# Kernel optimization log

Hardware: AMD Instinct MI355X
Metric: run time of the kernel (lower is better)

## Reference

```python
import jax, jax.numpy as jnp
import numpy as np

B, D, E = 16384, 2048, 16
MIN_K, MAX_K = 1, 4
H = D // 2  # hidden width of similarity/routing MLPs
TOP20 = int(0.2 * D)  # static: int(0.2 * x.shape[-1])


def _lin_init(k, fan_in, shape):
    bound = 1.0 / np.sqrt(fan_in)
    return jax.random.uniform(k, shape, jnp.float32, -bound, bound)


def setup_inputs() -> dict:
    key = jax.random.key(0)
    ks = jax.random.split(key, 16)
    return {
        'x': jax.random.normal(ks[0], (B, D), jnp.float32),
        'expert_patterns': jax.random.normal(ks[1], (E, D), jnp.float32),
        # similarity_network: Linear(D, D//2) -> ReLU -> Linear(D//2, E)
        'Ws1': _lin_init(ks[2], D, (D, H)), 'bs1': _lin_init(ks[3], D, (H,)),
        'Ws2': _lin_init(ks[4], H, (H, E)), 'bs2': _lin_init(ks[5], H, (E,)),
        # routing_network: Linear(D+E, D//2) -> ReLU -> (Dropout eval) -> Linear(D//2, E) -> Softmax
        'Wr1': _lin_init(ks[6], D + E, (D + E, H)), 'br1': _lin_init(ks[7], D + E, (H,)),
        'Wr2': _lin_init(ks[8], H, (H, E)), 'br2': _lin_init(ks[9], H, (E,)),
        # k_predictor: Linear(6,16) -> ReLU -> Linear(16,1) -> Sigmoid
        'Wk1': _lin_init(ks[10], 6, (6, 16)), 'bk1': _lin_init(ks[11], 6, (16,)),
        'Wk2': _lin_init(ks[12], 16, (16, 1)), 'bk2': _lin_init(ks[13], 16, (1,)),
    }


def _feature_analysis(x):
    mean = jnp.mean(x, axis=-1, keepdims=True)
    var_u = jnp.var(x, axis=-1, ddof=1)  # torch.var is unbiased
    std = jnp.sqrt(var_u[:, None] + 1e-8)
    skew = jnp.mean(((x - mean) / std) ** 3, axis=-1)
    ax = jnp.abs(x)
    sorted_ax = -jnp.sort(-ax, axis=-1)  # descending
    total = jnp.sum(sorted_ax, axis=-1)
    top = jnp.sum(sorted_ax[:, :TOP20], axis=-1)
    # stacked in DynamicTopKSelector order: sparsity,variance,magnitude,norm,skewness,concentration
    stats = jnp.stack([
        jnp.mean((x == 0).astype(jnp.float32), axis=-1),
        var_u,
        jnp.max(ax, axis=-1),
        jnp.linalg.norm(x, axis=-1),
        skew,
        top / (total + 1e-8),
    ], axis=-1)  # [B, 6]
    return stats


def _lower_median(v):
    # torch.median returns the lower of two middle elements for even n
    n = v.shape[0]
    return jnp.sort(v)[(n - 1) // 2]


def reference(x, expert_patterns, Ws1, bs1, Ws2, bs2, Wr1, br1, Wr2, br2, Wk1, bk1, Wk2, bk2):
    stats = _feature_analysis(x)  # [B, 6]
    # expert specialization
    sims = x @ expert_patterns.T                                  # [B, E]
    spec = jax.nn.relu(x @ Ws1 + bs1) @ Ws2 + bs2                 # [B, E]
    spec_scores = jax.nn.sigmoid(sims + spec)
    # routing network (dropout inactive in eval)
    ri = jnp.concatenate([x, spec_scores], axis=-1)               # [B, D+E]
    probs = jax.nn.softmax(jax.nn.relu(ri @ Wr1 + br1) @ Wr2 + br2, axis=-1)
    # dynamic top-k (host-side scalar in torch -> static-shape pad/mask here)
    k_ratio = jax.nn.sigmoid(jax.nn.relu(stats @ Wk1 + bk1) @ Wk2 + bk2)[:, 0]
    k_values = MIN_K + (MAX_K - MIN_K) * k_ratio
    k = jnp.clip(jnp.floor(_lower_median(k_values)).astype(jnp.int32), MIN_K, MAX_K)
    k = jax.lax.stop_gradient(k)
    topk_probs, topk_idx = jax.lax.top_k(probs, MAX_K)            # [B, MAX_K]
    mask = jnp.arange(MAX_K) < k                                  # first k slots active
    gates = jax.nn.softmax(jnp.where(mask, topk_probs, -1e30), axis=-1)
    return gates, topk_idx, probs, stats
```

## Files before the change

kernel.cpp:

```cpp
#include <hip/hip_runtime.h>
#include <hip/hip_bf16.h>

typedef unsigned short u16;
typedef __attribute__((ext_vector_type(8))) short bf16x8;
typedef __attribute__((ext_vector_type(4))) float f32x4;

#define BB 16384
#define DD 2048
#define KEXT 2112
#define HH 1024
#define EE 16
#define TOPN 409

__device__ __forceinline__ u16 f2bf(float f) {
    union { float f; unsigned u; } c; c.f = f;
    unsigned r = c.u + 0x7fffu + ((c.u >> 16) & 1u);
    return (u16)(r >> 16);
}
__device__ __forceinline__ float bf2f(u16 h) {
    union { unsigned u; float f; } c; c.u = ((unsigned)h) << 16; return c.f;
}

__device__ __forceinline__ void ld16_lds(const void* g, void* l) {
    __builtin_amdgcn_global_load_lds(
        (const __attribute__((address_space(1))) unsigned int*)g,
        (__attribute__((address_space(3))) unsigned int*)l, 16, 0, 0);
}

__global__ __launch_bounds__(256)
void prep_t(const float* __restrict__ Ws1, const float* __restrict__ Wr1,
            u16* __restrict__ w1t, u16* __restrict__ wr1h, u16* __restrict__ wr1l,
            const float* __restrict__ Ws2, const float* __restrict__ Wr2,
            const float* __restrict__ pat,
            u16* __restrict__ w2t1, u16* __restrict__ wr2th, u16* __restrict__ wr2tl,
            u16* __restrict__ patTh, u16* __restrict__ patTl)
{
    __shared__ float tile[64][65];
    const int kt = blockIdx.x;
    const int nt = blockIdx.y;
    const int mat = blockIdx.z;
    const int t = threadIdx.x;
    if (mat == 2) {
        int idx = (kt * 16 + nt) * 256 + t;
        if (idx < EE * HH) {
            int e = idx / HH, n = idx % HH;
            w2t1[idx] = f2bf(Ws2[(size_t)n * EE + e]);
            float v = Wr2[(size_t)n * EE + e];
            u16 h = f2bf(v);
            wr2th[idx] = h;
            wr2tl[idx] = f2bf(v - bf2f(h));
        }
        if (idx < EE * DD) {
            float v = pat[idx];
            u16 h = f2bf(v);
            patTh[idx] = h;
            patTl[idx] = f2bf(v - bf2f(h));
        }
        return;
    }
    if (mat == 0 && kt >= 32) return;
    const int k0 = kt * 64, n0 = nt * 64;
    const float* src = mat ? Wr1 : Ws1;
    const int kmax = mat ? (DD + EE) : DD;
    #pragma unroll
    for (int i = 0; i < 16; ++i) {
        int e = i * 256 + t;
        int r = e >> 6, c = e & 63;
        float v = (k0 + r < kmax) ? src[(size_t)(k0 + r) * HH + n0 + c] : 0.0f;
        tile[r][c] = v;
    }
    __syncthreads();
    #pragma unroll
    for (int i = 0; i < 16; ++i) {
        int e = i * 256 + t;
        int rn = e >> 6, ck = e & 63;
        float v = tile[ck][rn];
        size_t oidx = (size_t)(n0 + rn) * KEXT + k0 + ck;
        if (mat == 0) {
            w1t[oidx] = f2bf(v);
        } else {
            u16 h = f2bf(v);
            wr1h[oidx] = h;
            wr1l[oidx] = f2bf(v - bf2f(h));
        }
    }
}

__global__ __launch_bounds__(256)
void stats_kernel(const float* __restrict__ x,
                  const float* __restrict__ Wk1, const float* __restrict__ bk1,
                  const float* __restrict__ Wk2, const float* __restrict__ bk2,
                  float* __restrict__ stats_out, u16* __restrict__ xh, u16* __restrict__ xl,
                  unsigned* __restrict__ kflags)
{
    const int wid = threadIdx.x >> 6;
    const int lane = threadIdx.x & 63;
    const int row = blockIdx.x * 4 + wid;
    const float* xr = x + (size_t)row * DD;

    float v[32];
    #pragma unroll
    for (int s = 0; s < 8; ++s) {
        float4 a = *(const float4*)(xr + s * 256 + lane * 4);
        v[s*4+0]=a.x; v[s*4+1]=a.y; v[s*4+2]=a.z; v[s*4+3]=a.w;
    }

    u16* ph = xh + (size_t)row * KEXT;
    u16* pl = xl + (size_t)row * KEXT;
    #pragma unroll
    for (int s = 0; s < 8; ++s) {
        union { u16 a[4]; unsigned long long q; } H, L;
        #pragma unroll
        for (int c = 0; c < 4; ++c) {
            float f = v[s*4+c];
            u16 h = f2bf(f);
            H.a[c] = h; L.a[c] = f2bf(f - bf2f(h));
        }
        *(unsigned long long*)(ph + s*256 + lane*4) = H.q;
        *(unsigned long long*)(pl + s*256 + lane*4) = L.q;
    }
    ph[DD + lane] = 0;
    pl[DD + lane] = 0;

    float s1 = 0;
    #pragma unroll
    for (int j = 0; j < 32; ++j) s1 += v[j];
    #pragma unroll
    for (int off = 32; off >= 1; off >>= 1) s1 += __shfl_xor(s1, off);
    const float mean = s1 * (1.0f/2048.0f);

    float s2=0, s3=0, sa=0, sq=0, zc=0, mx=0;
    #pragma unroll
    for (int j = 0; j < 32; ++j) {
        float d = v[j] - mean;
        s2 += d*d; s3 += d*d*d;
        float av = fabsf(v[j]);
        sa += av; sq += v[j]*v[j];
        mx = fmaxf(mx, av);
        zc += (v[j] == 0.0f) ? 1.0f : 0.0f;
    }
    #pragma unroll
    for (int off = 32; off >= 1; off >>= 1) {
        s2 += __shfl_xor(s2, off);
        s3 += __shfl_xor(s3, off);
        sa += __shfl_xor(sa, off);
        sq += __shfl_xor(sq, off);
        zc += __shfl_xor(zc, off);
        mx = fmaxf(mx, __shfl_xor(mx, off));
    }

    #pragma unroll
    for (int j = 0; j < 32; ++j) v[j] = fabsf(v[j]);

    unsigned lo = 0, hi = 0x7F800000u;
    while (lo < hi) {
        unsigned mid = (lo + hi) >> 1;
        float midf = __uint_as_float(mid);
        unsigned cnt = 0;
        #pragma unroll
        for (int j = 0; j < 32; ++j)
            cnt += (unsigned)__popcll(__ballot(v[j] > midf));
        if (cnt < TOPN) hi = mid; else lo = mid + 1;
    }
    const float T = __uint_as_float(lo);

    float cg = 0, sg = 0;
    #pragma unroll
    for (int j = 0; j < 32; ++j) {
        if (v[j] > T) { cg += 1.0f; sg += v[j]; }
    }
    #pragma unroll
    for (int off = 32; off >= 1; off >>= 1) { cg += __shfl_xor(cg, off); sg += __shfl_xor(sg, off); }

    if (lane == 0) {
        float top = sg + ((float)TOPN - cg) * T;
        float var_u = s2 * (1.0f/2047.0f);
        float stdv = sqrtf(var_u + 1e-8f);
        float st0 = zc * (1.0f/2048.0f);
        float st1 = var_u;
        float st2 = mx;
        float st3 = sqrtf(sq);
        float st4 = (s3 * (1.0f/2048.0f)) / (stdv*stdv*stdv);
        float st5 = top / (sa + 1e-8f);
        float* so = stats_out + (size_t)row * 6;
        so[0]=st0; so[1]=st1; so[2]=st2; so[3]=st3; so[4]=st4; so[5]=st5;
        float stv[6] = {st0,st1,st2,st3,st4,st5};
        float o = bk2[0];
        #pragma unroll
        for (int i = 0; i < 16; ++i) {
            float h = bk1[i];
            #pragma unroll
            for (int f = 0; f < 6; ++f) h += stv[f] * Wk1[f*16 + i];
            o += fmaxf(h, 0.0f) * Wk2[i];
        }
        float kr = 1.0f / (1.0f + expf(-o));
        float kv = 1.0f + 3.0f * kr;
        kflags[row] = (kv < 2.0f ? 1u : 0u) | (kv < 3.0f ? 0x10000u : 0u);
    }
}

__global__ __launch_bounds__(1024)
void kmed_kernel(const unsigned* __restrict__ kflags, int* __restrict__ counters)
{
    const int t = threadIdx.x;
    unsigned s = 0;
    for (int i = t; i < BB; i += 1024) s += kflags[i];
    #pragma unroll
    for (int off = 32; off >= 1; off >>= 1) s += __shfl_xor(s, off);
    __shared__ unsigned red[16];
    if ((t & 63) == 0) red[t >> 6] = s;
    __syncthreads();
    if (t == 0) {
        unsigned tot = 0;
        #pragma unroll
        for (int w = 0; w < 16; ++w) tot += red[w];
        counters[0] = (int)(tot & 0xFFFFu);
        counters[1] = (int)(tot >> 16);
    }
}

template<bool SPLIT3, bool OSPLIT, bool FUSE_SPEC>
__global__ __launch_bounds__(256)
void gemm_tile(const u16* __restrict__ Ah, const u16* __restrict__ Al,
               const u16* __restrict__ Bh, const u16* __restrict__ Bl,
               const float* __restrict__ bias,
               u16* __restrict__ Oh, u16* __restrict__ Ol,
               const u16* __restrict__ w2t, float* __restrict__ spec_part,
               int kiters, int stride)
{
    __shared__ u16 SM[SPLIT3 ? 4*8192 : 2*8192];
    u16* AsH = SM;
    u16* BsH = SM + 8192;
    u16* AsL = SPLIT3 ? SM + 2*8192 : SM;
    u16* BsL = SPLIT3 ? SM + 3*8192 : SM;
    const int t = threadIdx.x;
    const int id = blockIdx.x;
    const int xcd = id & 7;
    const int jj = id >> 3;
    const int nblk = jj & 7;
    const int mgrp = jj >> 3;
    const int m0 = (xcd * 16 + mgrp) * 128;
    const int n0 = nblk * 128;
    const int wid = t >> 6, lane = t & 63, l16 = lane & 15, q = lane >> 4;
    const int wm = (wid & 1) * 64, wn = (wid >> 1) * 64;
    const int x7 = l16 & 7;

    f32x4 acc[4][4] = {};

    for (int it = 0; it < kiters; ++it) {
        const int k0 = it * 64;
        __syncthreads();
        #pragma unroll
        for (int s = 0; s < 4; ++s) {
            int seg = t + s * 256;
            int row = seg >> 3;
            int c = (seg & 7) ^ (row & 7);
            size_t goff = (size_t)k0 + c * 8;
            size_t aoff = (size_t)(m0 + row) * stride + goff;
            size_t boff = (size_t)(n0 + row) * stride + goff;
            ld16_lds(Ah + aoff, (void*)(AsH + seg * 8));
            ld16_lds(Bh + boff, (void*)(BsH + seg * 8));
            if constexpr (SPLIT3) {
                ld16_lds(Al + aoff, (void*)(AsL + seg * 8));
                ld16_lds(Bl + boff, (void*)(BsL + seg * 8));
            }
        }
        __syncthreads();
        #pragma unroll
        for (int h = 0; h < 2; ++h) {
            const int coff = ((4*h + q) ^ x7) * 8;
            bf16x8 afh[4], bfh[4], afl[4], bfl[4];
            #pragma unroll
            for (int i = 0; i < 4; ++i) {
                const int ra = (wm + 16*i + l16) * 64 + coff;
                const int rb = (wn + 16*i + l16) * 64 + coff;
                afh[i] = *(const bf16x8*)(AsH + ra);
                bfh[i] = *(const bf16x8*)(BsH + rb);
                if constexpr (SPLIT3) {
                    afl[i] = *(const bf16x8*)(AsL + ra);
                    bfl[i] = *(const bf16x8*)(BsL + rb);
                }
            }
            #pragma unroll
            for (int i = 0; i < 4; ++i)
                #pragma unroll
                for (int j = 0; j < 4; ++j) {
                    acc[i][j] = __builtin_amdgcn_mfma_f32_16x16x32_bf16(afh[i], bfh[j], acc[i][j], 0, 0, 0);
                    if constexpr (SPLIT3) {
                        acc[i][j] = __builtin_amdgcn_mfma_f32_16x16x32_bf16(afh[i], bfl[j], acc[i][j], 0, 0, 0);
                        acc[i][j] = __builtin_amdgcn_mfma_f32_16x16x32_bf16(afl[i], bfh[j], acc[i][j], 0, 0, 0);
                    }
                }
        }
    }

    if constexpr (FUSE_SPEC) {
        __syncthreads();
        u16* h1t = SM;
        #pragma unroll
        for (int j = 0; j < 4; ++j) {
            int col = wn + 16*j + l16;
            float bvj = bias[n0 + col];
            #pragma unroll
            for (int i = 0; i < 4; ++i)
                #pragma unroll
                for (int r = 0; r < 4; ++r) {
                    int row = wm + 16*i + q*4 + r;
                    float vv = acc[i][j][r] + bvj;
                    vv = vv > 0.0f ? vv : 0.0f;
                    h1t[row * 128 + col] = f2bf(vv);
                }
        }
        __syncthreads();
        const int mb = wid * 32;
        f32x4 s16[2] = {};
        #pragma unroll
        for (int kk = 0; kk < 4; ++kk) {
            bf16x8 wb = *(const bf16x8*)(w2t + (size_t)l16 * HH + n0 + kk*32 + q*8);
            #pragma unroll
            for (int i2 = 0; i2 < 2; ++i2) {
                bf16x8 af = *(const bf16x8*)(h1t + (mb + i2*16 + l16) * 128 + kk*32 + q*8);
                s16[i2] = __builtin_amdgcn_mfma_f32_16x16x32_bf16(af, wb, s16[i2], 0, 0, 0);
            }
        }
        #pragma unroll
        for (int i2 = 0; i2 < 2; ++i2)
            #pragma unroll
            for (int r = 0; r < 4; ++r) {
                int row = m0 + mb + i2*16 + q*4 + r;
                spec_part[((size_t)nblk * BB + row) * EE + l16] = s16[i2][r];
            }
    } else {
        #pragma unroll
        for (int j = 0; j < 4; ++j) {
            int col = n0 + wn + 16*j + l16;
            float bv = bias[col];
            #pragma unroll
            for (int i = 0; i < 4; ++i)
                #pragma unroll
                for (int r = 0; r < 4; ++r) {
                    int row = m0 + wm + 16*i + q*4 + r;
                    float vv = acc[i][j][r] + bv;
                    vv = vv > 0.0f ? vv : 0.0f;
                    u16 h = f2bf(vv);
                    Oh[(size_t)row * HH + col] = h;
                    if constexpr (OSPLIT) Ol[(size_t)row * HH + col] = f2bf(vv - bf2f(h));
                }
        }
    }
}

__global__ __launch_bounds__(256)
void thinA(const u16* __restrict__ xh, const u16* __restrict__ xl,
           const u16* __restrict__ patTh, const u16* __restrict__ patTl,
           const float* __restrict__ spec_part,
           const float* __restrict__ bs2,
           u16* __restrict__ xh_w, u16* __restrict__ xl_w)
{
    const int t = threadIdx.x;
    const int wid = t >> 6, lane = t & 63, l16 = lane & 15, q = lane >> 4;
    const int m0 = blockIdx.x * 16;
    f32x4 acc = {};
    for (int it = wid; it < 64; it += 4) {
        const int k0 = it * 32;
        bf16x8 a0 = *(const bf16x8*)(xh + (size_t)(m0 + l16) * KEXT + k0 + q*8);
        bf16x8 a1 = *(const bf16x8*)(xl + (size_t)(m0 + l16) * KEXT + k0 + q*8);
        bf16x8 b0 = *(const bf16x8*)(patTh + (size_t)l16 * DD + k0 + q*8);
        bf16x8 b1 = *(const bf16x8*)(patTl + (size_t)l16 * DD + k0 + q*8);
        acc = __builtin_amdgcn_mfma_f32_16x16x32_bf16(a0, b0, acc, 0, 0, 0);
        acc = __builtin_amdgcn_mfma_f32_16x16x32_bf16(a0, b1, acc, 0, 0, 0);
        acc = __builtin_amdgcn_mfma_f32_16x16x32_bf16(a1, b0, acc, 0, 0, 0);
    }
    __shared__ f32x4 red[4][64];
    red[wid][lane] = acc;
    __syncthreads();
    if (wid == 0) {
        f32x4 v = red[0][lane];
        #pragma unroll
        for (int w = 1; w < 4; ++w) {
            f32x4 o = red[w][lane];
            v[0]+=o[0]; v[1]+=o[1]; v[2]+=o[2]; v[3]+=o[3];
        }
        const float b2 = bs2[l16];
        #pragma unroll
        for (int r = 0; r < 4; ++r) {
            int row = m0 + q*4 + r;
            float sp = 0.0f;
            #pragma unroll
            for (int p = 0; p < 8; ++p)
                sp += spec_part[((size_t)p * BB + row) * EE + l16];
            float ssv = 1.0f / (1.0f + expf(-(v[r] + sp + b2)));
            u16 h = f2bf(ssv);
            u16 lo = f2bf(ssv - bf2f(h));
            xh_w[(size_t)row * KEXT + DD + l16] = h;
            xl_w[(size_t)row * KEXT + DD + l16] = lo;
        }
    }
}

__global__ __launch_bounds__(256)
void thinB(const u16* __restrict__ hh, const u16* __restrict__ hl,
           const u16* __restrict__ wr2th, const u16* __restrict__ wr2tl,
           const float* __restrict__ br2, const int* __restrict__ counters,
           float* __restrict__ out_gates, float* __restrict__ out_idx,
           float* __restrict__ out_probs)
{
    const int t = threadIdx.x;
    const int wid = t >> 6, lane = t & 63, l16 = lane & 15, q = lane >> 4;
    const int m0 = blockIdx.x * 16;
    f32x4 acc = {};
    for (int it = wid; it < 32; it += 4) {
        const int k0 = it * 32;
        bf16x8 a0 = *(const bf16x8*)(hh + (size_t)(m0 + l16) * HH + k0 + q*8);
        bf16x8 a1 = *(const bf16x8*)(hl + (size_t)(m0 + l16) * HH + k0 + q*8);
        bf16x8 b0 = *(const bf16x8*)(wr2th + (size_t)l16 * HH + k0 + q*8);
        bf16x8 b1 = *(const bf16x8*)(wr2tl + (size_t)l16 * HH + k0 + q*8);
        acc = __builtin_amdgcn_mfma_f32_16x16x32_bf16(a0, b0, acc, 0, 0, 0);
        acc = __builtin_amdgcn_mfma_f32_16x16x32_bf16(a0, b1, acc, 0, 0, 0);
        acc = __builtin_amdgcn_mfma_f32_16x16x32_bf16(a1, b0, acc, 0, 0, 0);
    }
    __shared__ f32x4 red[4][64];
    red[wid][lane] = acc;
    __syncthreads();
    if (wid != 0) return;
    f32x4 v = red[0][lane];
    #pragma unroll
    for (int w = 1; w < 4; ++w) {
        f32x4 o = red[w][lane];
        v[0]+=o[0]; v[1]+=o[1]; v[2]+=o[2]; v[3]+=o[3];
    }
    const float b2 = br2[l16];
    const int c2 = counters[0], c3 = counters[1];
    const int k = (c2 >= 8192) ? 1 : ((c3 >= 8192) ? 2 : 3);
    #pragma unroll
    for (int r = 0; r < 4; ++r) {
        const int row = m0 + q*4 + r;
        float lg = v[r] + b2;
        float mxv = lg;
        #pragma unroll
        for (int off = 1; off < 16; off <<= 1) mxv = fmaxf(mxv, __shfl_xor(mxv, off));
        float e = expf(lg - mxv);
        float den = e;
        #pragma unroll
        for (int off = 1; off < 16; off <<= 1) den += __shfl_xor(den, off);
        float p = e / den;
        out_probs[(size_t)row * EE + l16] = p;
        int kcur = (int)((__float_as_uint(p) & ~15u) | (15u - (unsigned)l16));
        float tv[4]; int ti[4];
        #pragma unroll
        for (int s = 0; s < 4; ++s) {
            int kk = kcur;
            #pragma unroll
            for (int off = 1; off < 16; off <<= 1) kk = max(kk, __shfl_xor(kk, off));
            int widx = 15 - (kk & 15);
            ti[s] = widx;
            tv[s] = __shfl(p, q * 16 + widx);
            if (l16 == widx) kcur = 0;
        }
        float den2 = 0.0f;
        float g[4];
        #pragma unroll
        for (int s = 0; s < 4; ++s) {
            g[s] = expf(tv[s] - tv[0]);
            if (s < k) den2 += g[s];
        }
        if (l16 < 4) {
            out_gates[(size_t)row * 4 + l16] = (l16 < k) ? g[l16] / den2 : 0.0f;
            out_idx[(size_t)row * 4 + l16] = (float)ti[l16];
        }
    }
}

extern "C" void kernel_launch(void* const* d_in, const int* in_sizes, int n_in,
                              void* d_out, int out_size, void* d_ws, size_t ws_size,
                              hipStream_t stream) {
    const float* x   = (const float*)d_in[0];
    const float* pat = (const float*)d_in[1];
    const float* Ws1 = (const float*)d_in[2];
    const float* bs1 = (const float*)d_in[3];
    const float* Ws2 = (const float*)d_in[4];
    const float* bs2 = (const float*)d_in[5];
    const float* Wr1 = (const float*)d_in[6];
    const float* br1 = (const float*)d_in[7];
    const float* Wr2 = (const float*)d_in[8];
    const float* br2 = (const float*)d_in[9];
    const float* Wk1 = (const float*)d_in[10];
    const float* bk1 = (const float*)d_in[11];
    const float* Wk2 = (const float*)d_in[12];
    const float* bk2 = (const float*)d_in[13];

    char* ws = (char*)d_ws;
    size_t off = 0;
    auto alloc = [&](size_t bytes) { char* p = ws + off; off += (bytes + 255) & ~(size_t)255; return p; };
    u16* xh     = (u16*)alloc((size_t)BB * KEXT * 2);
    u16* xl     = (u16*)alloc((size_t)BB * KEXT * 2);
    u16* w1t    = (u16*)alloc((size_t)HH * KEXT * 2);
    u16* wr1h   = (u16*)alloc((size_t)HH * KEXT * 2);
    u16* wr1l   = (u16*)alloc((size_t)HH * KEXT * 2);
    u16* w2t1   = (u16*)alloc((size_t)EE * HH * 2);
    u16* wr2th  = (u16*)alloc((size_t)EE * HH * 2);
    u16* wr2tl  = (u16*)alloc((size_t)EE * HH * 2);
    u16* patTh  = (u16*)alloc((size_t)EE * DD * 2);
    u16* patTl  = (u16*)alloc((size_t)EE * DD * 2);
    u16* ha     = (u16*)alloc((size_t)BB * HH * 2);
    u16* hb     = (u16*)alloc((size_t)BB * HH * 2);
    unsigned* kflags = (unsigned*)alloc((size_t)BB * 4);
    int* cnt      = (int*)alloc(64);

    float* spec_part = (float*)hb;

    float* out        = (float*)d_out;
    float* out_gates  = out;
    float* out_idx    = out + (size_t)BB * 4;
    float* out_probs  = out + (size_t)BB * 8;
    float* out_stats  = out + (size_t)BB * 24;

    prep_t<<<dim3(33, 16, 3), 256, 0, stream>>>(Ws1, Wr1, w1t, wr1h, wr1l,
        Ws2, Wr2, pat, w2t1, wr2th, wr2tl, patTh, patTl);

    stats_kernel<<<BB/4, 256, 0, stream>>>(x, Wk1, bk1, Wk2, bk2, out_stats, xh, xl, kflags);

    kmed_kernel<<<1, 1024, 0, stream>>>(kflags, cnt);

    gemm_tile<false, false, true><<<1024, 256, 0, stream>>>(
        xh, nullptr, w1t, nullptr, bs1, nullptr, nullptr, w2t1, spec_part, 32, KEXT);

    thinA<<<BB/16, 256, 0, stream>>>(xh, xl, patTh, patTl, spec_part, bs2, xh, xl);

    gemm_tile<true, true, false><<<1024, 256, 0, stream>>>(
        xh, xl, wr1h, wr1l, br1, ha, hb, nullptr, nullptr, 33, KEXT);

    thinB<<<BB/16, 256, 0, stream>>>(ha, hb, wr2th, wr2tl, br2, cnt,
                                     out_gates, out_idx, out_probs);
}
```

Baseline: 610.5 us.

## Fuse second routing layer and expert-similarity GEMV into the large GEMM epilogues

The routing GEMM now applies bias and ReLU, keeps the hidden tile in shared memory as a bf16 hi/lo split, and multiplies it by Wr2 in its epilogue, writing per-column-block partial logits. This removes the round trip of the 16384x1024 hidden activations through global memory. The x·patterns similarity GEMV moves into the first GEMM's K loop: each column block handles one eighth of K, using two waves, and reuses the A fragments already in registers. The thin kernels become small reductions over 8 partial sums. In exchange the main loop of the first GEMM gets extra uncoalesced global loads on some iterations, and more partial-sum buffers are written and read.

New measurement: 570.1 us. 1.07x faster.

```diff
diff --git a/kernel.cpp b/kernel.cpp
--- a/kernel.cpp
+++ b/kernel.cpp
@@ -219,20 +219,16 @@
     }
 }
 
-template<bool SPLIT3, bool OSPLIT, bool FUSE_SPEC>
 __global__ __launch_bounds__(256)
-void gemm_tile(const u16* __restrict__ Ah, const u16* __restrict__ Al,
-               const u16* __restrict__ Bh, const u16* __restrict__ Bl,
-               const float* __restrict__ bias,
-               u16* __restrict__ Oh, u16* __restrict__ Ol,
-               const u16* __restrict__ w2t, float* __restrict__ spec_part,
-               int kiters, int stride)
-{
-    __shared__ u16 SM[SPLIT3 ? 4*8192 : 2*8192];
+void gemm_h1(const u16* __restrict__ xh, const u16* __restrict__ xl,
+             const u16* __restrict__ w1t, const float* __restrict__ bias,
+             const u16* __restrict__ w2t,
+             const u16* __restrict__ patTh, const u16* __restrict__ patTl,
+             float* __restrict__ spec_part, float* __restrict__ sims_part)
+{
+    __shared__ u16 SM[2*8192];
     u16* AsH = SM;
     u16* BsH = SM + 8192;
-    u16* AsL = SPLIT3 ? SM + 2*8192 : SM;
-    u16* BsL = SPLIT3 ? SM + 3*8192 : SM;
     const int t = threadIdx.x;
     const int id = blockIdx.x;
     const int xcd = id & 7;
@@ -244,10 +240,12 @@
     const int wid = t >> 6, lane = t & 63, l16 = lane & 15, q = lane >> 4;
     const int wm = (wid & 1) * 64, wn = (wid >> 1) * 64;
     const int x7 = l16 & 7;
+    const bool swave = (wid < 2);
 
     f32x4 acc[4][4] = {};
-
-    for (int it = 0; it < kiters; ++it) {
+    f32x4 sacc[4] = {};
+
+    for (int it = 0; it < 32; ++it) {
         const int k0 = it * 64;
         __syncthreads();
         #pragma unroll
@@ -256,14 +254,127 @@
             int row = seg >> 3;
             int c = (seg & 7) ^ (row & 7);
             size_t goff = (size_t)k0 + c * 8;
-            size_t aoff = (size_t)(m0 + row) * stride + goff;
-            size_t boff = (size_t)(n0 + row) * stride + goff;
+            ld16_lds(xh  + (size_t)(m0 + row) * KEXT + goff, (void*)(AsH + seg * 8));
+            ld16_lds(w1t + (size_t)(n0 + row) * KEXT + goff, (void*)(BsH + seg * 8));
+        }
+        __syncthreads();
+        const bool simiter = ((it & 7) == nblk);
+        #pragma unroll
+        for (int h = 0; h < 2; ++h) {
+            const int coff = ((4*h + q) ^ x7) * 8;
+            bf16x8 afh[4], bfh[4];
+            #pragma unroll
+            for (int i = 0; i < 4; ++i) {
+                afh[i] = *(const bf16x8*)(AsH + (wm + 16*i + l16) * 64 + coff);
+                bfh[i] = *(const bf16x8*)(BsH + (wn + 16*i + l16) * 64 + coff);
+            }
+            #pragma unroll
+            for (int i = 0; i < 4; ++i)
+                #pragma unroll
+                for (int j = 0; j < 4; ++j)
+                    acc[i][j] = __builtin_amdgcn_mfma_f32_16x16x32_bf16(afh[i], bfh[j], acc[i][j], 0, 0, 0);
+            if (simiter && swave) {
+                const int gc = k0 + (4*h + q) * 8;
+                bf16x8 pb0 = *(const bf16x8*)(patTh + (size_t)l16 * DD + gc);
+                bf16x8 pb1 = *(const bf16x8*)(patTl + (size_t)l16 * DD + gc);
+                #pragma unroll
+                for (int i = 0; i < 4; ++i) {
+                    bf16x8 al = *(const bf16x8*)(xl + (size_t)(m0 + wm + 16*i + l16) * KEXT + gc);
+                    sacc[i] = __builtin_amdgcn_mfma_f32_16x16x32_bf16(afh[i], pb0, sacc[i], 0, 0, 0);
+                    sacc[i] = __builtin_amdgcn_mfma_f32_16x16x32_bf16(afh[i], pb1, sacc[i], 0, 0, 0);
+                    sacc[i] = __builtin_amdgcn_mfma_f32_16x16x32_bf16(al,     pb0, sacc[i], 0, 0, 0);
+                }
+            }
+        }
+    }
+
+    __syncthreads();
+    u16* h1t = SM;
+    #pragma unroll
+    for (int j = 0; j < 4; ++j) {
+        int col = wn + 16*j + l16;
+        float bvj = bias[n0 + col];
+        #pragma unroll
+        for (int i = 0; i < 4; ++i)
+            #pragma unroll
+            for (int r = 0; r < 4; ++r) {
+                int row = wm + 16*i + q*4 + r;
+                float vv = acc[i][j][r] + bvj;
+                vv = vv > 0.0f ? vv : 0.0f;
+                h1t[row * 128 + col] = f2bf(vv);
+            }
+    }
+    __syncthreads();
+    const int mb = wid * 32;
+    f32x4 s16[2] = {};
+    #pragma unroll
+    for (int kk = 0; kk < 4; ++kk) {
+        bf16x8 wb = *(const bf16x8*)(w2t + (size_t)l16 * HH + n0 + kk*32 + q*8);
+        #pragma unroll
+        for (int i2 = 0; i2 < 2; ++i2) {
+            bf16x8 af = *(const bf16x8*)(h1t + (mb + i2*16 + l16) * 128 + kk*32 + q*8);
+            s16[i2] = __builtin_amdgcn_mfma_f32_16x16x32_bf16(af, wb, s16[i2], 0, 0, 0);
+        }
+    }
+    #pragma unroll
+    for (int i2 = 0; i2 < 2; ++i2)
+        #pragma unroll
+        for (int r = 0; r < 4; ++r) {
+            int row = m0 + mb + i2*16 + q*4 + r;
+            spec_part[((size_t)nblk * BB + row) * EE + l16] = s16[i2][r];
+        }
+    if (swave) {
+        #pragma unroll
+        for (int i = 0; i < 4; ++i)
+            #pragma unroll
+            for (int r = 0; r < 4; ++r) {
+                int row = m0 + wm + 16*i + q*4 + r;
+                sims_part[((size_t)nblk * BB + row) * EE + l16] = sacc[i][r];
+            }
+    }
+}
+
+__global__ __launch_bounds__(256)
+void gemm_h2(const u16* __restrict__ Ah, const u16* __restrict__ Al,
+             const u16* __restrict__ Bh, const u16* __restrict__ Bl,
+             const float* __restrict__ bias,
+             const u16* __restrict__ wr2th, const u16* __restrict__ wr2tl,
+             float* __restrict__ lg_part)
+{
+    __shared__ u16 SM[4*8192];
+    u16* AsH = SM;
+    u16* BsH = SM + 8192;
+    u16* AsL = SM + 2*8192;
+    u16* BsL = SM + 3*8192;
+    const int t = threadIdx.x;
+    const int id = blockIdx.x;
+    const int xcd = id & 7;
+    const int jj = id >> 3;
+    const int nblk = jj & 7;
+    const int mgrp = jj >> 3;
+    const int m0 = (xcd * 16 + mgrp) * 128;
+    const int n0 = nblk * 128;
+    const int wid = t >> 6, lane = t & 63, l16 = lane & 15, q = lane >> 4;
+    const int wm = (wid & 1) * 64, wn = (wid >> 1) * 64;
+    const int x7 = l16 & 7;
+
+    f32x4 acc[4][4] = {};
+
+    for (int it = 0; it < 33; ++it) {
+        const int k0 = it * 64;
+        __syncthreads();
+        #pragma unroll
+        for (int s = 0; s < 4; ++s) {
+            int seg = t + s * 256;
+            int row = seg >> 3;
+            int c = (seg & 7) ^ (row & 7);
+            size_t goff = (size_t)k0 + c * 8;
+            size_t aoff = (size_t)(m0 + row) * KEXT + goff;
+            size_t boff = (size_t)(n0 + row) * KEXT + goff;
             ld16_lds(Ah + aoff, (void*)(AsH + seg * 8));
             ld16_lds(Bh + boff, (void*)(BsH + seg * 8));
-            if constexpr (SPLIT3) {
-                ld16_lds(Al + aoff, (void*)(AsL + seg * 8));
-                ld16_lds(Bl + boff, (void*)(BsL + seg * 8));
-            }
+            ld16_lds(Al + aoff, (void*)(AsL + seg * 8));
+            ld16_lds(Bl + boff, (void*)(BsL + seg * 8));
         }
         __syncthreads();
         #pragma unroll
@@ -276,166 +387,108 @@
                 const int rb = (wn + 16*i + l16) * 64 + coff;
                 afh[i] = *(const bf16x8*)(AsH + ra);
                 bfh[i] = *(const bf16x8*)(BsH + rb);
-                if constexpr (SPLIT3) {
-                    afl[i] = *(const bf16x8*)(AsL + ra);
-                    bfl[i] = *(const bf16x8*)(BsL + rb);
-                }
+                afl[i] = *(const bf16x8*)(AsL + ra);
+                bfl[i] = *(const bf16x8*)(BsL + rb);
             }
             #pragma unroll
             for (int i = 0; i < 4; ++i)
                 #pragma unroll
                 for (int j = 0; j < 4; ++j) {
                     acc[i][j] = __builtin_amdgcn_mfma_f32_16x16x32_bf16(afh[i], bfh[j], acc[i][j], 0, 0, 0);
-                    if constexpr (SPLIT3) {
-                        acc[i][j] = __builtin_amdgcn_mfma_f32_16x16x32_bf16(afh[i], bfl[j], acc[i][j], 0, 0, 0);
-                        acc[i][j] = __builtin_amdgcn_mfma_f32_16x16x32_bf16(afl[i], bfh[j], acc[i][j], 0, 0, 0);
-                    }
+                    acc[i][j] = __builtin_amdgcn_mfma_f32_16x16x32_bf16(afh[i], bfl[j], acc[i][j], 0, 0, 0);
+                    acc[i][j] = __builtin_amdgcn_mfma_f32_16x16x32_bf16(afl[i], bfh[j], acc[i][j], 0, 0, 0);
                 }
         }
     }
 
-    if constexpr (FUSE_SPEC) {
-        __syncthreads();
-        u16* h1t = SM;
-        #pragma unroll
-        for (int j = 0; j < 4; ++j) {
-            int col = wn + 16*j + l16;
-            float bvj = bias[n0 + col];
-            #pragma unroll
-            for (int i = 0; i < 4; ++i)
-                #pragma unroll
-                for (int r = 0; r < 4; ++r) {
-                    int row = wm + 16*i + q*4 + r;
-                    float vv = acc[i][j][r] + bvj;
-                    vv = vv > 0.0f ? vv : 0.0f;
-                    h1t[row * 128 + col] = f2bf(vv);
-                }
-        }
-        __syncthreads();
-        const int mb = wid * 32;
-        f32x4 s16[2] = {};
-        #pragma unroll
-        for (int kk = 0; kk < 4; ++kk) {
-            bf16x8 wb = *(const bf16x8*)(w2t + (size_t)l16 * HH + n0 + kk*32 + q*8);
-            #pragma unroll
-            for (int i2 = 0; i2 < 2; ++i2) {
-                bf16x8 af = *(const bf16x8*)(h1t + (mb + i2*16 + l16) * 128 + kk*32 + q*8);
-                s16[i2] = __builtin_amdgcn_mfma_f32_16x16x32_bf16(af, wb, s16[i2], 0, 0, 0);
+    __syncthreads();
+    u16* h2h = SM;
+    u16* h2l = SM + 16384;
+    #pragma unroll
+    for (int j = 0; j < 4; ++j) {
+        int col = wn + 16*j + l16;
+        float bvj = bias[n0 + col];
+        #pragma unroll
+        for (int i = 0; i < 4; ++i)
+            #pragma unroll
+            for (int r = 0; r < 4; ++r) {
+                int row = wm + 16*i + q*4 + r;
+                float vv = acc[i][j][r] + bvj;
+                vv = vv > 0.0f ? vv : 0.0f;
+                u16 h = f2bf(vv);
+                h2h[row * 128 + col] = h;
+                h2l[row * 128 + col] = f2bf(vv - bf2f(h));
             }
-        }
-        #pragma unroll
-        for (int i2 = 0; i2 < 2; ++i2)
-            #pragma unroll
-            for (int r = 0; r < 4; ++r) {
-                int row = m0 + mb + i2*16 + q*4 + r;
-                spec_part[((size_t)nblk * BB + row) * EE + l16] = s16[i2][r];
-            }
-    } else {
-        #pragma unroll
-        for (int j = 0; j < 4; ++j) {
-            int col = n0 + wn + 16*j + l16;
-            float bv = bias[col];
-            #pragma unroll
-            for (int i = 0; i < 4; ++i)
-                #pragma unroll
-                for (int r = 0; r < 4; ++r) {
-                    int row = m0 + wm + 16*i + q*4 + r;
-                    float vv = acc[i][j][r] + bv;
-                    vv = vv > 0.0f ? vv : 0.0f;
-                    u16 h = f2bf(vv);
-                    Oh[(size_t)row * HH + col] = h;
-                    if constexpr (OSPLIT) Ol[(size_t)row * HH + col] = f2bf(vv - bf2f(h));
-                }
-        }
-    }
-}
-
-__global__ __launch_bounds__(256)
-void thinA(const u16* __restrict__ xh, const u16* __restrict__ xl,
-           const u16* __restrict__ patTh, const u16* __restrict__ patTl,
-           const float* __restrict__ spec_part,
-           const float* __restrict__ bs2,
-           u16* __restrict__ xh_w, u16* __restrict__ xl_w)
-{
-    const int t = threadIdx.x;
-    const int wid = t >> 6, lane = t & 63, l16 = lane & 15, q = lane >> 4;
+    }
+    __syncthreads();
+    const int mb = wid * 32;
+    f32x4 lacc[2] = {};
+    #pragma unroll
+    for (int kk = 0; kk < 4; ++kk) {
+        bf16x8 wbh = *(const bf16x8*)(wr2th + (size_t)l16 * HH + n0 + kk*32 + q*8);
+        bf16x8 wbl = *(const bf16x8*)(wr2tl + (size_t)l16 * HH + n0 + kk*32 + q*8);
+        #pragma unroll
+        for (int i2 = 0; i2 < 2; ++i2) {
+            bf16x8 ah = *(const bf16x8*)(h2h + (mb + i2*16 + l16) * 128 + kk*32 + q*8);
+            bf16x8 al = *(const bf16x8*)(h2l + (mb + i2*16 + l16) * 128 + kk*32 + q*8);
+            lacc[i2] = __builtin_amdgcn_mfma_f32_16x16x32_bf16(ah, wbh, lacc[i2], 0, 0, 0);
+            lacc[i2] = __builtin_amdgcn_mfma_f32_16x16x32_bf16(ah, wbl, lacc[i2], 0, 0, 0);
+            lacc[i2] = __builtin_amdgcn_mfma_f32_16x16x32_bf16(al, wbh, lacc[i2], 0, 0, 0);
+        }
+    }
+    #pragma unroll
+    for (int i2 = 0; i2 < 2; ++i2)
+        #pragma unroll
+        for (int r = 0; r < 4; ++r) {
+            int row = m0 + mb + i2*16 + q*4 + r;
+            lg_part[((size_t)nblk * BB + row) * EE + l16] = lacc[i2][r];
+        }
+}
+
+__global__ __launch_bounds__(64)
+void thinAc(const float* __restrict__ spec_part, const float* __restrict__ sims_part,
+            const float* __restrict__ bs2,
+            u16* __restrict__ xh_w, u16* __restrict__ xl_w)
+{
+    const int lane = threadIdx.x & 63;
+    const int l16 = lane & 15, q = lane >> 4;
     const int m0 = blockIdx.x * 16;
-    f32x4 acc = {};
-    for (int it = wid; it < 64; it += 4) {
-        const int k0 = it * 32;
-        bf16x8 a0 = *(const bf16x8*)(xh + (size_t)(m0 + l16) * KEXT + k0 + q*8);
-        bf16x8 a1 = *(const bf16x8*)(xl + (size_t)(m0 + l16) * KEXT + k0 + q*8);
-        bf16x8 b0 = *(const bf16x8*)(patTh + (size_t)l16 * DD + k0 + q*8);
-        bf16x8 b1 = *(const bf16x8*)(patTl + (size_t)l16 * DD + k0 + q*8);
-        acc = __builtin_amdgcn_mfma_f32_16x16x32_bf16(a0, b0, acc, 0, 0, 0);
-        acc = __builtin_amdgcn_mfma_f32_16x16x32_bf16(a0, b1, acc, 0, 0, 0);
-        acc = __builtin_amdgcn_mfma_f32_16x16x32_bf16(a1, b0, acc, 0, 0, 0);
-    }
-    __shared__ f32x4 red[4][64];
-    red[wid][lane] = acc;
-    __syncthreads();
-    if (wid == 0) {
-        f32x4 v = red[0][lane];
-        #pragma unroll
-        for (int w = 1; w < 4; ++w) {
-            f32x4 o = red[w][lane];
-            v[0]+=o[0]; v[1]+=o[1]; v[2]+=o[2]; v[3]+=o[3];
-        }
-        const float b2 = bs2[l16];
-        #pragma unroll
-        for (int r = 0; r < 4; ++r) {
-            int row = m0 + q*4 + r;
-            float sp = 0.0f;
-            #pragma unroll
-            for (int p = 0; p < 8; ++p)
-                sp += spec_part[((size_t)p * BB + row) * EE + l16];
-            float ssv = 1.0f / (1.0f + expf(-(v[r] + sp + b2)));
-            u16 h = f2bf(ssv);
-            u16 lo = f2bf(ssv - bf2f(h));
-            xh_w[(size_t)row * KEXT + DD + l16] = h;
-            xl_w[(size_t)row * KEXT + DD + l16] = lo;
-        }
-    }
-}
-
-__global__ __launch_bounds__(256)
-void thinB(const u16* __restrict__ hh, const u16* __restrict__ hl,
-           const u16* __restrict__ wr2th, const u16* __restrict__ wr2tl,
-           const float* __restrict__ br2, const int* __restrict__ counters,
-           float* __restrict__ out_gates, float* __restrict__ out_idx,
-           float* __restrict__ out_probs)
-{
-    const int t = threadIdx.x;
-    const int wid = t >> 6, lane = t & 63, l16 = lane & 15, q = lane >> 4;
+    const float b2 = bs2[l16];
+    #pragma unroll
+    for (int r = 0; r < 4; ++r) {
+        int row = m0 + q*4 + r;
+        float sp = 0.0f;
+        #pragma unroll
+        for (int p = 0; p < 8; ++p) {
+            sp += spec_part[((size_t)p * BB + row) * EE + l16];
+            sp += sims_part[((size_t)p * BB + row) * EE + l16];
+        }
+        float ssv = 1.0f / (1.0f + expf(-(sp + b2)));
+        u16 h = f2bf(ssv);
+        xh_w[(size_t)row * KEXT + DD + l16] = h;
+        xl_w[(size_t)row * KEXT + DD + l16] = f2bf(ssv - bf2f(h));
+    }
+}
+
+__global__ __launch_bounds__(64)
+void thinBc(const float* __restrict__ lg_part,
+            const float* __restrict__ br2, const int* __restrict__ counters,
+            float* __restrict__ out_gates, float* __restrict__ out_idx,
+            float* __restrict__ out_probs)
+{
+    const int lane = threadIdx.x & 63;
+    const int l16 = lane & 15, q = lane >> 4;
     const int m0 = blockIdx.x * 16;
-    f32x4 acc = {};
-    for (int it = wid; it < 32; it += 4) {
-        const int k0 = it * 32;
-        bf16x8 a0 = *(const bf16x8*)(hh + (size_t)(m0 + l16) * HH + k0 + q*8);
-        bf16x8 a1 = *(const bf16x8*)(hl + (size_t)(m0 + l16) * HH + k0 + q*8);
-        bf16x8 b0 = *(const bf16x8*)(wr2th + (size_t)l16 * HH + k0 + q*8);
-        bf16x8 b1 = *(const bf16x8*)(wr2tl + (size_t)l16 * HH + k0 + q*8);
-        acc = __builtin_amdgcn_mfma_f32_16x16x32_bf16(a0, b0, acc, 0, 0, 0);
-        acc = __builtin_amdgcn_mfma_f32_16x16x32_bf16(a0, b1, acc, 0, 0, 0);
-        acc = __builtin_amdgcn_mfma_f32_16x16x32_bf16(a1, b0, acc, 0, 0, 0);
-    }
-    __shared__ f32x4 red[4][64];
-    red[wid][lane] = acc;
-    __syncthreads();
-    if (wid != 0) return;
-    f32x4 v = red[0][lane];
-    #pragma unroll
-    for (int w = 1; w < 4; ++w) {
-        f32x4 o = red[w][lane];
-        v[0]+=o[0]; v[1]+=o[1]; v[2]+=o[2]; v[3]+=o[3];
-    }
     const float b2 = br2[l16];
     const int c2 = counters[0], c3 = counters[1];
     const int k = (c2 >= 8192) ? 1 : ((c3 >= 8192) ? 2 : 3);
     #pragma unroll
     for (int r = 0; r < 4; ++r) {
         const int row = m0 + q*4 + r;
-        float lg = v[r] + b2;
+        float lg = b2;
+        #pragma unroll
+        for (int p = 0; p < 8; ++p)
+            lg += lg_part[((size_t)p * BB + row) * EE + l16];
         float mxv = lg;
         #pragma unroll
         for (int off = 1; off < 16; off <<= 1) mxv = fmaxf(mxv, __shfl_xor(mxv, off));
@@ -502,12 +555,14 @@
     u16* wr2tl  = (u16*)alloc((size_t)EE * HH * 2);
     u16* patTh  = (u16*)alloc((size_t)EE * DD * 2);
     u16* patTl  = (u16*)alloc((size_t)EE * DD * 2);
-    u16* ha     = (u16*)alloc((size_t)BB * HH * 2);
-    u16* hb     = (u16*)alloc((size_t)BB * HH * 2);
+    float* partA = (float*)alloc((size_t)16 * BB * EE * 4);
+    float* partB = (float*)alloc((size_t)8  * BB * EE * 4);
     unsigned* kflags = (unsigned*)alloc((size_t)BB * 4);
     int* cnt      = (int*)alloc(64);
 
-    float* spec_part = (float*)hb;
+    float* spec_part = partA;
+    float* sims_part = partA + (size_t)8 * BB * EE;
+    float* lg_part   = partB;
 
     float* out        = (float*)d_out;
     float* out_gates  = out;
@@ -522,14 +577,12 @@
 
     kmed_kernel<<<1, 1024, 0, stream>>>(kflags, cnt);
 
-    gemm_tile<false, false, true><<<1024, 256, 0, stream>>>(
-        xh, nullptr, w1t, nullptr, bs1, nullptr, nullptr, w2t1, spec_part, 32, KEXT);
-
-    thinA<<<BB/16, 256, 0, stream>>>(xh, xl, patTh, patTl, spec_part, bs2, xh, xl);
-
-    gemm_tile<true, true, false><<<1024, 256, 0, stream>>>(
-        xh, xl, wr1h, wr1l, br1, ha, hb, nullptr, nullptr, 33, KEXT);
-
-    thinB<<<BB/16, 256, 0, stream>>>(ha, hb, wr2th, wr2tl, br2, cnt,
-                                     out_gates, out_idx, out_probs);
-}
+    gemm_h1<<<1024, 256, 0, stream>>>(xh, xl, w1t, bs1, w2t1, patTh, patTl,
+                                      spec_part, sims_part);
+
+    thinAc<<<BB/16, 64, 0, stream>>>(spec_part, sims_part, bs2, xh, xl);
+
+    gemm_h2<<<1024, 256, 0, stream>>>(xh, xl, wr1h, wr1l, br1, wr2th, wr2tl, lg_part);
+
+    thinBc<<<BB/16, 64, 0, stream>>>(lg_part, br2, cnt, out_gates, out_idx, out_probs);
+}
```
